# Kernel tuning notes

Measured on AMD Instinct MI355X. Metric: run time of the kernel, lower is better.

## Reference

```python
import jax, jax.numpy as jnp
import numpy as np

N_NODES = 100000
N_EDGES = 3200000
IN_DIM = 256
HID = 64
OUT_DIM = 1


def gcn_conv(x, W, b, src, dst, n):
    # PyG GCNConv: h = x @ W; add self loops; sym-normalize; aggregate; + b
    h = x @ W  # [N, F]
    # degrees include self loops (edge_weight = 1), computed on target nodes
    ones = jnp.ones(src.shape[0], dtype=x.dtype)
    deg = jax.ops.segment_sum(ones, dst, num_segments=n) + 1.0  # +1 for self loop
    dinv = jax.lax.rsqrt(deg)
    norm = dinv[src] * dinv[dst]  # [E]
    msg = h[src] * norm[:, None]  # gather + scale
    out = jax.ops.segment_sum(msg, dst, num_segments=n)
    # self-loop contribution: norm_ii = dinv[i]^2
    out = out + h * (dinv * dinv)[:, None]
    return out + b


def setup_inputs() -> dict:
    key = jax.random.key(0)
    ks = jax.random.split(key, 6)
    x = jax.random.normal(ks[0], (N_NODES, IN_DIM), dtype=jnp.float32)
    edge_index = jax.random.randint(ks[1], (2, N_EDGES), 0, N_NODES, dtype=jnp.int64)
    W1 = jax.random.normal(ks[2], (IN_DIM, HID), dtype=jnp.float32) / np.sqrt(IN_DIM)
    b1 = jnp.zeros((HID,), dtype=jnp.float32)
    W2 = jax.random.normal(ks[3], (HID, HID), dtype=jnp.float32) / np.sqrt(HID)
    b2 = jnp.zeros((HID,), dtype=jnp.float32)
    Wf = jax.random.normal(ks[4], (HID, OUT_DIM), dtype=jnp.float32) / np.sqrt(HID)
    bf = jnp.zeros((OUT_DIM,), dtype=jnp.float32)
    return {"x": x, "edge_index": edge_index, "W1": W1, "b1": b1,
            "W2": W2, "b2": b2, "Wf": Wf, "bf": bf}


def reference(x, edge_index, W1, b1, W2, b2, Wf, bf):
    src, dst = edge_index[0], edge_index[1]
    n = x.shape[0]
    h = jax.nn.relu(gcn_conv(x, W1, b1, src, dst, n))
    h = jax.nn.relu(gcn_conv(h, W2, b2, src, dst, n))
    g = jnp.mean(h, axis=0)  # [HID] graph readout
    return jax.nn.sigmoid(g @ Wf + bf)  # [OUT_DIM]
```

## Files before the change

### kernel.cpp

```cpp
#include <hip/hip_runtime.h>


typedef unsigned int u32;
typedef unsigned short u16;
typedef unsigned char u8;
typedef short s16x8 __attribute__((ext_vector_type(8)));
typedef __bf16 bf16x8 __attribute__((ext_vector_type(8)));
typedef float f32x4 __attribute__((ext_vector_type(4)));

constexpr int HID  = 64;
constexpr int SH   = 7;
constexpr int BK   = 128;
constexpr int BPAD = 1024;
constexpr int CH   = 4096;
constexpr int SLOT = 5120;
constexpr int NBLK2 = 4096;

static __device__ __forceinline__ u8 f2fp8(float f) {
    int p = __builtin_amdgcn_cvt_pk_fp8_f32(f, f, 0, false);
    return (u8)(p & 0xFF);
}
static __device__ __forceinline__ float fp82f(u8 v) {
    return __builtin_amdgcn_cvt_f32_fp8((int)v, 0);
}
static __device__ __forceinline__ u16 f2bf(float f) {
    u32 u = __float_as_uint(f);
    return (u16)((u + 0x7FFFu + ((u >> 16) & 1u)) >> 16);
}

__global__ void init_bcur_kernel(int* __restrict__ bcur, int B) {
    int b = blockIdx.x * 256 + threadIdx.x;
    if (b < B) bcur[b] = b * SLOT;
}

__global__ __launch_bounds__(256) void partition_kernel(const int* __restrict__ src,
                                                        const int* __restrict__ dst,
                                                        int* __restrict__ bcur,
                                                        u32* __restrict__ ep, int ne) {
    __shared__ int hcnt[BPAD];
    __shared__ int hoff[BPAD];
    __shared__ int gbase[BPAD];
    __shared__ u32 stage[CH];
    __shared__ int ssc[256];
    const int t = threadIdx.x;
    const int base = blockIdx.x * CH;
    const int cnt = min(CH, ne - base);
    for (int i = t; i < BPAD; i += 256) hcnt[i] = 0;
    __syncthreads();

    int myr[CH / 256];
    #pragma unroll
    for (int k = 0; k < CH / 256; ++k) {
        int i = t + k * 256;
        if (i < cnt) myr[k] = atomicAdd(&hcnt[dst[base + i] >> SH], 1);
    }
    __syncthreads();
    {
        int c0 = hcnt[t*4], c1 = hcnt[t*4+1], c2 = hcnt[t*4+2], c3 = hcnt[t*4+3];
        int tsum = c0 + c1 + c2 + c3;
        ssc[t] = tsum; __syncthreads();
        int run = tsum;
        for (int off = 1; off < 256; off <<= 1) {
            int v = (t >= off) ? ssc[t - off] : 0;
            __syncthreads();
            run += v; ssc[t] = run;
            __syncthreads();
        }
        int ex = run - tsum;
        hoff[t*4] = ex; ex += c0;
        hoff[t*4+1] = ex; ex += c1;
        hoff[t*4+2] = ex; ex += c2;
        hoff[t*4+3] = ex;
    }
    __syncthreads();
    for (int b = t; b < BPAD; b += 256) {
        int c = hcnt[b];
        if (c) gbase[b] = atomicAdd(&bcur[b], c);
    }
    #pragma unroll
    for (int k = 0; k < CH / 256; ++k) {
        int i = t + k * 256;
        if (i < cnt) {
            int s = src[base + i], d = dst[base + i];
            stage[hoff[d >> SH] + myr[k]] = ((u32)(d & (BK - 1)) << 20) | (u32)s;
        }
    }
    __syncthreads();
    for (int i = t; i < cnt; i += 256) {
        u32 v = stage[i];
        int lo = 0;
        #pragma unroll
        for (int s = 512; s; s >>= 1) {
            int m = lo + s;
            if (m < BPAD && hoff[m] <= i) lo = m;
        }
        ep[gbase[lo] + (i - hoff[lo])] = v;
    }
}

__global__ __launch_bounds__(256) void bucket_sort_kernel(const u32* __restrict__ ep,
                                                          const int* __restrict__ bcur,
                                                          int* __restrict__ eidx,
                                                          int* __restrict__ rowend,
                                                          float* __restrict__ dinv, int n) {
    __shared__ int cnt[BK];
    __shared__ int sc[BK];
    __shared__ int cur[BK];
    const int t = threadIdx.x, b = blockIdx.x;
    const int beg = b * SLOT, end = bcur[b];
    if (t < BK) cnt[t] = 0;
    __syncthreads();
    for (int p = beg + t; p < end; p += 256) atomicAdd(&cnt[ep[p] >> 20], 1);
    __syncthreads();
    if (t < BK) sc[t] = cnt[t];
    __syncthreads();
    for (int o = 1; o < BK; o <<= 1) {
        int v = 0;
        if (t < BK && t >= o) v = sc[t - o];
        __syncthreads();
        if (t < BK) sc[t] += v;
        __syncthreads();
    }
    if (t < BK) {
        int node = b * BK + t;
        if (node < n) {
            rowend[node] = beg + sc[t];
            dinv[node] = rsqrtf((float)cnt[t] + 1.0f);
        }
        cur[t] = beg + sc[t] - cnt[t];
    }
    __syncthreads();
    for (int p = beg + t; p < end; p += 256) {
        u32 v = ep[p];
        int r = atomicAdd(&cur[v >> 20], 1);
        eidx[r] = (int)(v & 0xFFFFFu);
    }
}

template <int K>
__global__ void pack_w_kernel(const float* __restrict__ W, u16* __restrict__ wpack) {
    int i = blockIdx.x * 256 + threadIdx.x;
    if (i >= K * 64) return;
    int e = i & 7, lane = (i >> 3) & 63, nt = (i >> 9) & 3, kk = i >> 11;
    int k = kk * 32 + (lane >> 4) * 8 + e;
    int c = nt * 16 + (lane & 15);
    wpack[i] = f2bf(W[k * HID + c]);
}

template <int K, typename TIn>
__global__ __launch_bounds__(256) void mfma_gemm_kernel(const TIn* __restrict__ A,
                                                        const u16* __restrict__ wpack,
                                                        const float* __restrict__ dinv,
                                                        u8* __restrict__ out8, int n) {
    const int t = threadIdx.x;
    const int lane = t & 63;
    const int wid = t >> 6;
    const int r16 = lane & 15;
    const int kgrp = lane >> 4;
    const int ntiles = (n + 15) >> 4;
    for (int tile = blockIdx.x * 4 + wid; tile < ntiles; tile += gridDim.x * 4) {
        const int row0 = tile * 16;
        const int arow = row0 + r16;
        f32x4 acc[4] = {f32x4{0,0,0,0}, f32x4{0,0,0,0}, f32x4{0,0,0,0}, f32x4{0,0,0,0}};
        #pragma unroll
        for (int kk = 0; kk < K / 32; ++kk) {
            s16x8 abits;
            if constexpr (sizeof(TIn) == 4) {
                const float* Af = (const float*)A;
                if (arow < n) {
                    const float4* p0 = (const float4*)(Af + (size_t)arow * K + kk * 32 + kgrp * 8);
                    float4 v0 = p0[0], v1 = p0[1];
                    abits[0] = (short)f2bf(v0.x); abits[1] = (short)f2bf(v0.y);
                    abits[2] = (short)f2bf(v0.z); abits[3] = (short)f2bf(v0.w);
                    abits[4] = (short)f2bf(v1.x); abits[5] = (short)f2bf(v1.y);
                    abits[6] = (short)f2bf(v1.z); abits[7] = (short)f2bf(v1.w);
                } else {
                    #pragma unroll
                    for (int j = 0; j < 8; ++j) abits[j] = 0;
                }
            } else {
                const u8* Ab = (const u8*)A;
                u32 w0 = 0, w1 = 0;
                if (arow < n) {
                    const u32* p0 = (const u32*)(Ab + (size_t)arow * K + kk * 32 + kgrp * 8);
                    w0 = p0[0]; w1 = p0[1];
                }
                abits[0] = (short)f2bf(__builtin_amdgcn_cvt_f32_fp8((int)w0, 0));
                abits[1] = (short)f2bf(__builtin_amdgcn_cvt_f32_fp8((int)w0, 1));
                abits[2] = (short)f2bf(__builtin_amdgcn_cvt_f32_fp8((int)w0, 2));
                abits[3] = (short)f2bf(__builtin_amdgcn_cvt_f32_fp8((int)w0, 3));
                abits[4] = (short)f2bf(__builtin_amdgcn_cvt_f32_fp8((int)w1, 0));
                abits[5] = (short)f2bf(__builtin_amdgcn_cvt_f32_fp8((int)w1, 1));
                abits[6] = (short)f2bf(__builtin_amdgcn_cvt_f32_fp8((int)w1, 2));
                abits[7] = (short)f2bf(__builtin_amdgcn_cvt_f32_fp8((int)w1, 3));
            }
            bf16x8 afrag = __builtin_bit_cast(bf16x8, abits);
            const u16* wp = wpack + ((size_t)(kk * 4) * 64 + lane) * 8;
            #pragma unroll
            for (int nt = 0; nt < 4; ++nt) {
                bf16x8 bfrag = *(const bf16x8*)(wp + (size_t)nt * 64 * 8);
                acc[nt] = __builtin_amdgcn_mfma_f32_16x16x32_bf16(afrag, bfrag, acc[nt], 0, 0, 0);
            }
        }
        #pragma unroll
        for (int reg = 0; reg < 4; ++reg) {
            int r = row0 + kgrp * 4 + reg;
            if (r < n) {
                float dv = dinv[r];
                #pragma unroll
                for (int nt = 0; nt < 4; ++nt)
                    out8[(size_t)r * HID + nt * 16 + r16] = f2fp8(acc[nt][reg] * dv);
            }
        }
    }
}

#define CVT4(acc0, acc1, acc2, acc3, wv) \
    acc0 += __builtin_amdgcn_cvt_f32_fp8((int)(wv), 0); \
    acc1 += __builtin_amdgcn_cvt_f32_fp8((int)(wv), 1); \
    acc2 += __builtin_amdgcn_cvt_f32_fp8((int)(wv), 2); \
    acc3 += __builtin_amdgcn_cvt_f32_fp8((int)(wv), 3);

__global__ __launch_bounds__(256) void agg_csr_kernel(const u8* __restrict__ hp,
                                                      const int* __restrict__ eidx,
                                                      const int* __restrict__ rowend,
                                                      const float* __restrict__ dinv,
                                                      const float* __restrict__ bias,
                                                      u8* __restrict__ out, int n) {
    int w = (blockIdx.x * 256 + threadIdx.x) >> 6;
    int lane = threadIdx.x & 63;
    if (w >= n) return;
    const int g = lane >> 4, fb = lane & 15;
    int beg = (w & (BK - 1)) ? rowend[w - 1] : (w >> SH) * SLOT;
    int end = rowend[w];
    float a0 = 0.f, a1 = 0.f, a2 = 0.f, a3 = 0.f;
    int p = beg;
    for (; p + 32 <= end; p += 32) {
        int s[8];
        #pragma unroll
        for (int j = 0; j < 8; ++j) s[j] = __builtin_nontemporal_load(eidx + p + j * 4 + g);
        u32 wv[8];
        #pragma unroll
        for (int j = 0; j < 8; ++j) wv[j] = *(const u32*)(hp + (size_t)s[j] * 64 + fb * 4);
        #pragma unroll
        for (int j = 0; j < 8; ++j) { CVT4(a0, a1, a2, a3, wv[j]) }
    }
    if (p + 16 <= end) {
        int s[4];
        #pragma unroll
        for (int j = 0; j < 4; ++j) s[j] = __builtin_nontemporal_load(eidx + p + j * 4 + g);
        u32 wv[4];
        #pragma unroll
        for (int j = 0; j < 4; ++j) wv[j] = *(const u32*)(hp + (size_t)s[j] * 64 + fb * 4);
        #pragma unroll
        for (int j = 0; j < 4; ++j) { CVT4(a0, a1, a2, a3, wv[j]) }
        p += 16;
    }
    for (; p < end; p += 4) {
        int idx = p + g;
        bool valid = idx < end;
        int s = __builtin_nontemporal_load(eidx + (valid ? idx : beg));
        u32 wv = *(const u32*)(hp + (size_t)s * 64 + fb * 4);
        if (valid) { CVT4(a0, a1, a2, a3, wv) }
    }
    a0 += __shfl_xor(a0, 16); a0 += __shfl_xor(a0, 32);
    a1 += __shfl_xor(a1, 16); a1 += __shfl_xor(a1, 32);
    a2 += __shfl_xor(a2, 16); a2 += __shfl_xor(a2, 32);
    a3 += __shfl_xor(a3, 16); a3 += __shfl_xor(a3, 32);
    u32 sv = *(const u32*)(hp + (size_t)w * 64 + fb * 4);
    float dv = dinv[w];
    float v0 = fmaxf(dv * (a0 + __builtin_amdgcn_cvt_f32_fp8((int)sv, 0)) + bias[fb * 4 + 0], 0.f);
    float v1 = fmaxf(dv * (a1 + __builtin_amdgcn_cvt_f32_fp8((int)sv, 1)) + bias[fb * 4 + 1], 0.f);
    float v2 = fmaxf(dv * (a2 + __builtin_amdgcn_cvt_f32_fp8((int)sv, 2)) + bias[fb * 4 + 2], 0.f);
    float v3 = fmaxf(dv * (a3 + __builtin_amdgcn_cvt_f32_fp8((int)sv, 3)) + bias[fb * 4 + 3], 0.f);
    if (g == 0) {
        int r = __builtin_amdgcn_cvt_pk_fp8_f32(v0, v1, 0, false);
        r = __builtin_amdgcn_cvt_pk_fp8_f32(v2, v3, r, true);
        *(u32*)(out + (size_t)w * 64 + fb * 4) = (u32)r;
    }
}

__global__ __launch_bounds__(256) void agg_csr_reduce_kernel(const u8* __restrict__ hp,
                                                             const int* __restrict__ eidx,
                                                             const int* __restrict__ rowend,
                                                             const float* __restrict__ dinv,
                                                             const float* __restrict__ bias,
                                                             float* __restrict__ partials, int n) {
    __shared__ float sred[256];
    int t = threadIdx.x, lane = t & 63;
    const int g = lane >> 4, fb = lane & 15;
    int wid = (blockIdx.x * 256 + t) >> 6;
    int wstride = gridDim.x * 4;
    float bl0 = bias[fb * 4 + 0], bl1 = bias[fb * 4 + 1];
    float bl2 = bias[fb * 4 + 2], bl3 = bias[fb * 4 + 3];
    float t0 = 0.f, t1 = 0.f, t2 = 0.f, t3 = 0.f;
    for (int w = wid; w < n; w += wstride) {
        int beg = (w & (BK - 1)) ? rowend[w - 1] : (w >> SH) * SLOT;
        int end = rowend[w];
        float a0 = 0.f, a1 = 0.f, a2 = 0.f, a3 = 0.f;
        int p = beg;
        for (; p + 32 <= end; p += 32) {
            int s[8];
            #pragma unroll
            for (int j = 0; j < 8; ++j) s[j] = __builtin_nontemporal_load(eidx + p + j * 4 + g);
            u32 wv[8];
            #pragma unroll
            for (int j = 0; j < 8; ++j) wv[j] = *(const u32*)(hp + (size_t)s[j] * 64 + fb * 4);
            #pragma unroll
            for (int j = 0; j < 8; ++j) { CVT4(a0, a1, a2, a3, wv[j]) }
        }
        if (p + 16 <= end) {
            int s[4];
            #pragma unroll
            for (int j = 0; j < 4; ++j) s[j] = __builtin_nontemporal_load(eidx + p + j * 4 + g);
            u32 wv[4];
            #pragma unroll
            for (int j = 0; j < 4; ++j) wv[j] = *(const u32*)(hp + (size_t)s[j] * 64 + fb * 4);
            #pragma unroll
            for (int j = 0; j < 4; ++j) { CVT4(a0, a1, a2, a3, wv[j]) }
            p += 16;
        }
        for (; p < end; p += 4) {
            int idx = p + g;
            bool valid = idx < end;
            int s = __builtin_nontemporal_load(eidx + (valid ? idx : beg));
            u32 wv = *(const u32*)(hp + (size_t)s * 64 + fb * 4);
            if (valid) { CVT4(a0, a1, a2, a3, wv) }
        }
        a0 += __shfl_xor(a0, 16); a0 += __shfl_xor(a0, 32);
        a1 += __shfl_xor(a1, 16); a1 += __shfl_xor(a1, 32);
        a2 += __shfl_xor(a2, 16); a2 += __shfl_xor(a2, 32);
        a3 += __shfl_xor(a3, 16); a3 += __shfl_xor(a3, 32);
        u32 sv = *(const u32*)(hp + (size_t)w * 64 + fb * 4);
        float dv = dinv[w];
        t0 += fmaxf(dv * (a0 + __builtin_amdgcn_cvt_f32_fp8((int)sv, 0)) + bl0, 0.f);
        t1 += fmaxf(dv * (a1 + __builtin_amdgcn_cvt_f32_fp8((int)sv, 1)) + bl1, 0.f);
        t2 += fmaxf(dv * (a2 + __builtin_amdgcn_cvt_f32_fp8((int)sv, 2)) + bl2, 0.f);
        t3 += fmaxf(dv * (a3 + __builtin_amdgcn_cvt_f32_fp8((int)sv, 3)) + bl3, 0.f);
    }
    int wv_ = t >> 6;
    if (g == 0) {
        sred[wv_ * 64 + fb * 4 + 0] = t0;
        sred[wv_ * 64 + fb * 4 + 1] = t1;
        sred[wv_ * 64 + fb * 4 + 2] = t2;
        sred[wv_ * 64 + fb * 4 + 3] = t3;
    }
    __syncthreads();
    if (t < 64) partials[blockIdx.x * 64 + t] = sred[t] + sred[t + 64] + sred[t + 128] + sred[t + 192];
}

__global__ __launch_bounds__(256) void gsum_stage_kernel(const float* __restrict__ parts, int nblk,
                                                         float* __restrict__ gsum) {
    __shared__ float sred[256];
    int t = threadIdx.x, col = t & 63;
    float a = 0.f;
    for (int bk = blockIdx.x * 4 + (t >> 6); bk < nblk; bk += gridDim.x * 4)
        a += parts[bk * 64 + col];
    sred[t] = a; __syncthreads();
    if (t < 64) atomicAdd(&gsum[t], sred[t] + sred[t + 64] + sred[t + 128] + sred[t + 192]);
}

__global__ void final_gsum_kernel(const float* __restrict__ gsum, const float* __restrict__ Wf,
                                  const float* __restrict__ bf_, float* __restrict__ out, float invn) {
    int lane = threadIdx.x;
    float v = gsum[lane] * invn * Wf[lane];
    #pragma unroll
    for (int off = 32; off; off >>= 1) v += __shfl_down(v, off);
    if (lane == 0) out[0] = 1.f / (1.f + expf(-(v + bf_[0])));
}

template <int K, typename TIn>
__global__ __launch_bounds__(256) void gemm_scale_kernel(const TIn* __restrict__ A,
                                                         const float* __restrict__ W,
                                                         const float* __restrict__ dinv,
                                                         u8* __restrict__ out8, int n) {
    __shared__ float xs[16][K];
    const int t = threadIdx.x;
    const int row0 = blockIdx.x * 16;
    if constexpr (sizeof(TIn) == 4) {
        const float* Af = (const float*)A;
        for (int i = t; i < 16 * K; i += 256) {
            int r = i / K;
            (&xs[0][0])[i] = (row0 + r < n) ? Af[(size_t)row0 * K + i] : 0.f;
        }
    } else {
        const u8* Ab = (const u8*)A;
        for (int i = t; i < 16 * K; i += 256) {
            int r = i / K;
            (&xs[0][0])[i] = (row0 + r < n) ? fp82f(Ab[(size_t)row0 * K + i]) : 0.f;
        }
    }
    __syncthreads();
    const int c = t & 63, rg = t >> 6;
    float acc[4] = {0.f, 0.f, 0.f, 0.f};
    #pragma unroll 4
    for (int k = 0; k < K; ++k) {
        float w = W[k * HID + c];
        #pragma unroll
        for (int j = 0; j < 4; ++j) acc[j] += xs[rg + 4 * j][k] * w;
    }
    #pragma unroll
    for (int j = 0; j < 4; ++j) {
        int r = row0 + rg + 4 * j;
        if (r < n) out8[(size_t)r * HID + c] = f2fp8(acc[j] * dinv[r]);
    }
}
__global__ void deg_f_kernel(const int* __restrict__ dst, float* __restrict__ deg, int ne) {
    int i = blockIdx.x * blockDim.x + threadIdx.x, st = gridDim.x * blockDim.x;
    for (; i < ne; i += st) atomicAdd(&deg[dst[i]], 1.0f);
}
__global__ void dinvf_kernel(float* __restrict__ deg, int n) {
    int i = blockIdx.x * blockDim.x + threadIdx.x;
    if (i < n) deg[i] = rsqrtf(deg[i] + 1.0f);
}
__global__ __launch_bounds__(256) void aggregate_atomic_kernel(const u8* __restrict__ hp,
        const int* __restrict__ src, const int* __restrict__ dst,
        const float* __restrict__ dinv, float* __restrict__ outf, int ne) {
    size_t tt = (size_t)blockIdx.x * 256 + threadIdx.x;
    int e = (int)(tt >> 6), f = (int)(tt & 63);
    if (e >= ne) return;
    int s = src[e], d = dst[e];
    atomicAdd(&outf[(size_t)d * HID + f], fp82f(hp[s * HID + f]) * dinv[d]);
}
__global__ void finalize1_fb_kernel(u8* __restrict__ hp, const float* __restrict__ agg,
                                    const float* __restrict__ dinv, const float* __restrict__ b, int n) {
    size_t i = (size_t)blockIdx.x * blockDim.x + threadIdx.x;
    if (i >= (size_t)n * HID) return;
    int node = (int)(i >> 6);
    float v = agg[i] + fp82f(hp[i]) * dinv[node] + b[i & 63];
    hp[i] = f2fp8(fmaxf(v, 0.f));
}
__global__ __launch_bounds__(256) void finalize2_fb_kernel(const u8* __restrict__ hp,
        const float* __restrict__ agg, const float* __restrict__ dinv,
        const float* __restrict__ b, float* __restrict__ gsum, int n) {
    __shared__ float sred[256];
    const int t = threadIdx.x, c = t & 63;
    const size_t total = (size_t)n * HID;
    const size_t stride = (size_t)gridDim.x * blockDim.x;
    float acc = 0.f;
    for (size_t i = (size_t)blockIdx.x * blockDim.x + t; i < total; i += stride) {
        int node = (int)(i >> 6);
        acc += fmaxf(agg[i] + fp82f(hp[i]) * dinv[node] + b[c], 0.f);
    }
    sred[t] = acc; __syncthreads();
    if (t < 64) atomicAdd(&gsum[c], sred[t] + sred[t + 64] + sred[t + 128] + sred[t + 192]);
}
__global__ void final_gsum_fb_kernel(const float* __restrict__ gsum, const float* __restrict__ Wf,
                                     const float* __restrict__ bf_, float* __restrict__ out, int n) {
    int lane = threadIdx.x;
    float v = (gsum[lane] / (float)n) * Wf[lane];
    #pragma unroll
    for (int off = 32; off; off >>= 1) v += __shfl_down(v, off);
    if (lane == 0) out[0] = 1.f / (1.f + expf(-(v + bf_[0])));
}

extern "C" void kernel_launch(void* const* d_in, const int* in_sizes, int n_in,
                              void* d_out, int out_size, void* d_ws, size_t ws_size,
                              hipStream_t stream) {
    const float* x  = (const float*)d_in[0];
    const int*   ei = (const int*)d_in[1];
    const float* W1 = (const float*)d_in[2];
    const float* b1 = (const float*)d_in[3];
    const float* W2 = (const float*)d_in[4];
    const float* b2 = (const float*)d_in[5];
    const float* Wf = (const float*)d_in[6];
    const float* bf_ = (const float*)d_in[7];
    float* out = (float*)d_out;

    const int n  = in_sizes[0] / 256;
    const int ne = in_sizes[1] / 2;
    const int* srcp = ei;
    const int* dstp = ei + ne;
    const int B = (n + BK - 1) / BK;

    char* p = (char*)d_ws;
    u32*   ep     = (u32*)p;   p += ((size_t)B * SLOT + 4096) * 4;
    int*   bcur   = (int*)p;   p += BPAD * 4;
    float* dinv   = (float*)p; p += (size_t)n * 4;
    int*   rowend = (int*)p;   p += (size_t)n * 4;
    float* gsum   = (float*)p; p += 64 * 4;
    int*   eidx   = (int*)p;   p += ((size_t)B * SLOT + 4096) * 4;
    float* parts  = (float*)p; p += (size_t)NBLK2 * 64 * 4;
    p = (char*)(((uintptr_t)p + 15) & ~(uintptr_t)15);
    u16*   wpack1 = (u16*)p;   p += 256 * 64 * 2;
    u16*   wpack2 = (u16*)p;   p += 64 * 64 * 2;
    u8*    hp     = (u8*)p;    p += (size_t)n * HID;
    u8*    h1     = (u8*)p;    p += (size_t)n * HID;
    size_t need = (size_t)(p - (char*)d_ws);

    bool slack_ok = ((size_t)ne / (size_t)B) <= (size_t)(SLOT - 1024);

    if (ws_size >= need && n <= (1 << 17) && slack_ok) {
        (void)hipMemsetAsync(gsum, 0, 64 * 4, stream);
        init_bcur_kernel<<<(B + 255) / 256, 256, 0, stream>>>(bcur, B);
        partition_kernel<<<(ne + CH - 1) / CH, 256, 0, stream>>>(srcp, dstp, bcur, ep, ne);
        bucket_sort_kernel<<<B, 256, 0, stream>>>(ep, bcur, eidx, rowend, dinv, n);
        pack_w_kernel<256><<<64, 256, 0, stream>>>(W1, wpack1);
        pack_w_kernel<64><<<16, 256, 0, stream>>>(W2, wpack2);

        const int ntiles = (n + 15) / 16;
        const int gblk = (ntiles + 3) / 4;
        mfma_gemm_kernel<256, float><<<gblk, 256, 0, stream>>>(x, wpack1, dinv, hp, n);
        agg_csr_kernel<<<(n + 3) / 4, 256, 0, stream>>>(hp, eidx, rowend, dinv, b1, h1, n);
        mfma_gemm_kernel<64, u8><<<gblk, 256, 0, stream>>>(h1, wpack2, dinv, hp, n);
        agg_csr_reduce_kernel<<<NBLK2, 256, 0, stream>>>(hp, eidx, rowend, dinv, b2, parts, n);
        gsum_stage_kernel<<<128, 256, 0, stream>>>(parts, NBLK2, gsum);
        final_gsum_kernel<<<1, 64, 0, stream>>>(gsum, Wf, bf_, out, 1.0f / (float)n);
    } else {
        char* q = (char*)d_ws;
        float* dinvF = (float*)q; q += (size_t)n * 4;
        float* gsumF = (float*)q; q += 64 * 4;
        u8*    hpF   = (u8*)q;   q += (size_t)n * HID;
        float* aggF  = (float*)q;

        (void)hipMemsetAsync(dinvF, 0, ((size_t)n + 64) * 4, stream);
        deg_f_kernel<<<2048, 256, 0, stream>>>(dstp, dinvF, ne);
        dinvf_kernel<<<(n + 255) / 256, 256, 0, stream>>>(dinvF, n);

        gemm_scale_kernel<256, float><<<(n + 15) / 16, 256, 0, stream>>>(x, W1, dinvF, hpF, n);
        (void)hipMemsetAsync(aggF, 0, (size_t)n * HID * 4, stream);
        aggregate_atomic_kernel<<<(int)(((size_t)ne * 64 + 255) / 256), 256, 0, stream>>>(hpF, srcp, dstp, dinvF, aggF, ne);
        finalize1_fb_kernel<<<(int)(((size_t)n * HID + 255) / 256), 256, 0, stream>>>(hpF, aggF, dinvF, b1, n);

        gemm_scale_kernel<64, u8><<<(n + 15) / 16, 256, 0, stream>>>(hpF, W2, dinvF, hpF, n);
        (void)hipMemsetAsync(aggF, 0, (size_t)n * HID * 4, stream);
        aggregate_atomic_kernel<<<(int)(((size_t)ne * 64 + 255) / 256), 256, 0, stream>>>(hpF, srcp, dstp, dinvF, aggF, ne);
        finalize2_fb_kernel<<<2048, 256, 0, stream>>>(hpF, aggF, dinvF, b2, gsumF, n);
        final_gsum_fb_kernel<<<1, 64, 0, stream>>>(gsumF, Wf, bf_, out, n);
    }
}
```

Measured before the change: 267.9 us.

## Split feature matrices into two 32-column halves and aggregate each half separately

The hidden features are stored as two separate 32-byte-per-node FP8 arrays, and each aggregation pass runs twice, once per half. This shrinks the gathered working set of each pass (3.2 MB instead of 6.4 MB) so the random neighbor gathers fit better in cache. The trade-off is reading the CSR edge indices twice, launching extra kernels, and issuing 32-byte gathers that use less of each cache line. The GEMM kernels and the reduction stage are adapted to read and write the split layout.

```diff
diff --git a/kernel.cpp b/kernel.cpp
--- a/kernel.cpp
+++ b/kernel.cpp
@@ -149,9 +149,11 @@
 
 template <int K, typename TIn>
 __global__ __launch_bounds__(256) void mfma_gemm_kernel(const TIn* __restrict__ A,
+                                                        const TIn* __restrict__ A2,
                                                         const u16* __restrict__ wpack,
                                                         const float* __restrict__ dinv,
-                                                        u8* __restrict__ out8, int n) {
+                                                        u8* __restrict__ outA,
+                                                        u8* __restrict__ outB, int n) {
     const int t = threadIdx.x;
     const int lane = t & 63;
     const int wid = t >> 6;
@@ -179,10 +181,10 @@
                     for (int j = 0; j < 8; ++j) abits[j] = 0;
                 }
             } else {
-                const u8* Ab = (const u8*)A;
+                const u8* src = (kk == 0) ? (const u8*)A : (const u8*)A2;
                 u32 w0 = 0, w1 = 0;
                 if (arow < n) {
-                    const u32* p0 = (const u32*)(Ab + (size_t)arow * K + kk * 32 + kgrp * 8);
+                    const u32* p0 = (const u32*)(src + (size_t)arow * 32 + kgrp * 8);
                     w0 = p0[0]; w1 = p0[1];
                 }
                 abits[0] = (short)f2bf(__builtin_amdgcn_cvt_f32_fp8((int)w0, 0));
@@ -208,8 +210,10 @@
             if (r < n) {
                 float dv = dinv[r];
                 #pragma unroll
-                for (int nt = 0; nt < 4; ++nt)
-                    out8[(size_t)r * HID + nt * 16 + r16] = f2fp8(acc[nt][reg] * dv);
+                for (int nt = 0; nt < 4; ++nt) {
+                    u8* o = (nt < 2) ? outA : outB;
+                    o[(size_t)r * 32 + (nt & 1) * 16 + r16] = f2fp8(acc[nt][reg] * dv);
+                }
             }
         }
     }
@@ -221,78 +225,67 @@
     acc2 += __builtin_amdgcn_cvt_f32_fp8((int)(wv), 2); \
     acc3 += __builtin_amdgcn_cvt_f32_fp8((int)(wv), 3);
 
-__global__ __launch_bounds__(256) void agg_csr_kernel(const u8* __restrict__ hp,
-                                                      const int* __restrict__ eidx,
-                                                      const int* __restrict__ rowend,
-                                                      const float* __restrict__ dinv,
-                                                      const float* __restrict__ bias,
-                                                      u8* __restrict__ out, int n) {
+__global__ __launch_bounds__(256) void agg_half_kernel(const u8* __restrict__ hpH,
+                                                       const int* __restrict__ eidx,
+                                                       const int* __restrict__ rowend,
+                                                       const float* __restrict__ dinv,
+                                                       const float* __restrict__ biasH,
+                                                       u8* __restrict__ outH, int n) {
     int w = (blockIdx.x * 256 + threadIdx.x) >> 6;
     int lane = threadIdx.x & 63;
     if (w >= n) return;
-    const int g = lane >> 4, fb = lane & 15;
+    const int g = lane >> 3, fb = lane & 7;
     int beg = (w & (BK - 1)) ? rowend[w - 1] : (w >> SH) * SLOT;
     int end = rowend[w];
     float a0 = 0.f, a1 = 0.f, a2 = 0.f, a3 = 0.f;
     int p = beg;
     for (; p + 32 <= end; p += 32) {
-        int s[8];
-        #pragma unroll
-        for (int j = 0; j < 8; ++j) s[j] = __builtin_nontemporal_load(eidx + p + j * 4 + g);
-        u32 wv[8];
-        #pragma unroll
-        for (int j = 0; j < 8; ++j) wv[j] = *(const u32*)(hp + (size_t)s[j] * 64 + fb * 4);
-        #pragma unroll
-        for (int j = 0; j < 8; ++j) { CVT4(a0, a1, a2, a3, wv[j]) }
-    }
-    if (p + 16 <= end) {
         int s[4];
         #pragma unroll
-        for (int j = 0; j < 4; ++j) s[j] = __builtin_nontemporal_load(eidx + p + j * 4 + g);
+        for (int j = 0; j < 4; ++j) s[j] = __builtin_nontemporal_load(eidx + p + j * 8 + g);
         u32 wv[4];
         #pragma unroll
-        for (int j = 0; j < 4; ++j) wv[j] = *(const u32*)(hp + (size_t)s[j] * 64 + fb * 4);
+        for (int j = 0; j < 4; ++j) wv[j] = *(const u32*)(hpH + (size_t)s[j] * 32 + fb * 4);
         #pragma unroll
         for (int j = 0; j < 4; ++j) { CVT4(a0, a1, a2, a3, wv[j]) }
-        p += 16;
-    }
-    for (; p < end; p += 4) {
+    }
+    for (; p < end; p += 8) {
         int idx = p + g;
         bool valid = idx < end;
         int s = __builtin_nontemporal_load(eidx + (valid ? idx : beg));
-        u32 wv = *(const u32*)(hp + (size_t)s * 64 + fb * 4);
+        u32 wv = *(const u32*)(hpH + (size_t)s * 32 + fb * 4);
         if (valid) { CVT4(a0, a1, a2, a3, wv) }
     }
-    a0 += __shfl_xor(a0, 16); a0 += __shfl_xor(a0, 32);
-    a1 += __shfl_xor(a1, 16); a1 += __shfl_xor(a1, 32);
-    a2 += __shfl_xor(a2, 16); a2 += __shfl_xor(a2, 32);
-    a3 += __shfl_xor(a3, 16); a3 += __shfl_xor(a3, 32);
-    u32 sv = *(const u32*)(hp + (size_t)w * 64 + fb * 4);
+    a0 += __shfl_xor(a0, 8); a0 += __shfl_xor(a0, 16); a0 += __shfl_xor(a0, 32);
+    a1 += __shfl_xor(a1, 8); a1 += __shfl_xor(a1, 16); a1 += __shfl_xor(a1, 32);
+    a2 += __shfl_xor(a2, 8); a2 += __shfl_xor(a2, 16); a2 += __shfl_xor(a2, 32);
+    a3 += __shfl_xor(a3, 8); a3 += __shfl_xor(a3, 16); a3 += __shfl_xor(a3, 32);
+    u32 sv = *(const u32*)(hpH + (size_t)w * 32 + fb * 4);
     float dv = dinv[w];
-    float v0 = fmaxf(dv * (a0 + __builtin_amdgcn_cvt_f32_fp8((int)sv, 0)) + bias[fb * 4 + 0], 0.f);
-    float v1 = fmaxf(dv * (a1 + __builtin_amdgcn_cvt_f32_fp8((int)sv, 1)) + bias[fb * 4 + 1], 0.f);
-    float v2 = fmaxf(dv * (a2 + __builtin_amdgcn_cvt_f32_fp8((int)sv, 2)) + bias[fb * 4 + 2], 0.f);
-    float v3 = fmaxf(dv * (a3 + __builtin_amdgcn_cvt_f32_fp8((int)sv, 3)) + bias[fb * 4 + 3], 0.f);
+    float v0 = fmaxf(dv * (a0 + __builtin_amdgcn_cvt_f32_fp8((int)sv, 0)) + biasH[fb * 4 + 0], 0.f);
+    float v1 = fmaxf(dv * (a1 + __builtin_amdgcn_cvt_f32_fp8((int)sv, 1)) + biasH[fb * 4 + 1], 0.f);
+    float v2 = fmaxf(dv * (a2 + __builtin_amdgcn_cvt_f32_fp8((int)sv, 2)) + biasH[fb * 4 + 2], 0.f);
+    float v3 = fmaxf(dv * (a3 + __builtin_amdgcn_cvt_f32_fp8((int)sv, 3)) + biasH[fb * 4 + 3], 0.f);
     if (g == 0) {
         int r = __builtin_amdgcn_cvt_pk_fp8_f32(v0, v1, 0, false);
         r = __builtin_amdgcn_cvt_pk_fp8_f32(v2, v3, r, true);
-        *(u32*)(out + (size_t)w * 64 + fb * 4) = (u32)r;
-    }
-}
-
-__global__ __launch_bounds__(256) void agg_csr_reduce_kernel(const u8* __restrict__ hp,
-                                                             const int* __restrict__ eidx,
-                                                             const int* __restrict__ rowend,
-                                                             const float* __restrict__ dinv,
-                                                             const float* __restrict__ bias,
-                                                             float* __restrict__ partials, int n) {
-    __shared__ float sred[256];
+        __builtin_nontemporal_store((u32)r, (u32*)(outH + (size_t)w * 32 + fb * 4));
+    }
+}
+
+__global__ __launch_bounds__(256) void agg_reduce_half_kernel(const u8* __restrict__ hpH,
+                                                              const int* __restrict__ eidx,
+                                                              const int* __restrict__ rowend,
+                                                              const float* __restrict__ dinv,
+                                                              const float* __restrict__ biasH,
+                                                              float* __restrict__ partialsH, int n) {
+    __shared__ float sred[128];
     int t = threadIdx.x, lane = t & 63;
-    const int g = lane >> 4, fb = lane & 15;
+    const int g = lane >> 3, fb = lane & 7;
     int wid = (blockIdx.x * 256 + t) >> 6;
     int wstride = gridDim.x * 4;
-    float bl0 = bias[fb * 4 + 0], bl1 = bias[fb * 4 + 1];
-    float bl2 = bias[fb * 4 + 2], bl3 = bias[fb * 4 + 3];
+    float bl0 = biasH[fb * 4 + 0], bl1 = biasH[fb * 4 + 1];
+    float bl2 = biasH[fb * 4 + 2], bl3 = biasH[fb * 4 + 3];
     float t0 = 0.f, t1 = 0.f, t2 = 0.f, t3 = 0.f;
     for (int w = wid; w < n; w += wstride) {
         int beg = (w & (BK - 1)) ? rowend[w - 1] : (w >> SH) * SLOT;
@@ -300,38 +293,27 @@
         float a0 = 0.f, a1 = 0.f, a2 = 0.f, a3 = 0.f;
         int p = beg;
         for (; p + 32 <= end; p += 32) {
-            int s[8];
-            #pragma unroll
-            for (int j = 0; j < 8; ++j) s[j] = __builtin_nontemporal_load(eidx + p + j * 4 + g);
-            u32 wv[8];
-            #pragma unroll
-            for (int j = 0; j < 8; ++j) wv[j] = *(const u32*)(hp + (size_t)s[j] * 64 + fb * 4);
-            #pragma unroll
-            for (int j = 0; j < 8; ++j) { CVT4(a0, a1, a2, a3, wv[j]) }
-        }
-        if (p + 16 <= end) {
             int s[4];
             #pragma unroll
-            for (int j = 0; j < 4; ++j) s[j] = __builtin_nontemporal_load(eidx + p + j * 4 + g);
+            for (int j = 0; j < 4; ++j) s[j] = __builtin_nontemporal_load(eidx + p + j * 8 + g);
             u32 wv[4];
             #pragma unroll
-            for (int j = 0; j < 4; ++j) wv[j] = *(const u32*)(hp + (size_t)s[j] * 64 + fb * 4);
+            for (int j = 0; j < 4; ++j) wv[j] = *(const u32*)(hpH + (size_t)s[j] * 32 + fb * 4);
             #pragma unroll
             for (int j = 0; j < 4; ++j) { CVT4(a0, a1, a2, a3, wv[j]) }
-            p += 16;
-        }
-        for (; p < end; p += 4) {
+        }
+        for (; p < end; p += 8) {
             int idx = p + g;
             bool valid = idx < end;
             int s = __builtin_nontemporal_load(eidx + (valid ? idx : beg));
-            u32 wv = *(const u32*)(hp + (size_t)s * 64 + fb * 4);
+            u32 wv = *(const u32*)(hpH + (size_t)s * 32 + fb * 4);
             if (valid) { CVT4(a0, a1, a2, a3, wv) }
         }
-        a0 += __shfl_xor(a0, 16); a0 += __shfl_xor(a0, 32);
-        a1 += __shfl_xor(a1, 16); a1 += __shfl_xor(a1, 32);
-        a2 += __shfl_xor(a2, 16); a2 += __shfl_xor(a2, 32);
-        a3 += __shfl_xor(a3, 16); a3 += __shfl_xor(a3, 32);
-        u32 sv = *(const u32*)(hp + (size_t)w * 64 + fb * 4);
+        a0 += __shfl_xor(a0, 8); a0 += __shfl_xor(a0, 16); a0 += __shfl_xor(a0, 32);
+        a1 += __shfl_xor(a1, 8); a1 += __shfl_xor(a1, 16); a1 += __shfl_xor(a1, 32);
+        a2 += __shfl_xor(a2, 8); a2 += __shfl_xor(a2, 16); a2 += __shfl_xor(a2, 32);
+        a3 += __shfl_xor(a3, 8); a3 += __shfl_xor(a3, 16); a3 += __shfl_xor(a3, 32);
+        u32 sv = *(const u32*)(hpH + (size_t)w * 32 + fb * 4);
         float dv = dinv[w];
         t0 += fmaxf(dv * (a0 + __builtin_amdgcn_cvt_f32_fp8((int)sv, 0)) + bl0, 0.f);
         t1 += fmaxf(dv * (a1 + __builtin_amdgcn_cvt_f32_fp8((int)sv, 1)) + bl1, 0.f);
@@ -340,22 +322,25 @@
     }
     int wv_ = t >> 6;
     if (g == 0) {
-        sred[wv_ * 64 + fb * 4 + 0] = t0;
-        sred[wv_ * 64 + fb * 4 + 1] = t1;
-        sred[wv_ * 64 + fb * 4 + 2] = t2;
-        sred[wv_ * 64 + fb * 4 + 3] = t3;
-    }
-    __syncthreads();
-    if (t < 64) partials[blockIdx.x * 64 + t] = sred[t] + sred[t + 64] + sred[t + 128] + sred[t + 192];
-}
-
-__global__ __launch_bounds__(256) void gsum_stage_kernel(const float* __restrict__ parts, int nblk,
+        sred[wv_ * 32 + fb * 4 + 0] = t0;
+        sred[wv_ * 32 + fb * 4 + 1] = t1;
+        sred[wv_ * 32 + fb * 4 + 2] = t2;
+        sred[wv_ * 32 + fb * 4 + 3] = t3;
+    }
+    __syncthreads();
+    if (t < 32) partialsH[blockIdx.x * 32 + t] = sred[t] + sred[t + 32] + sred[t + 64] + sred[t + 96];
+}
+
+__global__ __launch_bounds__(256) void gsum_stage_kernel(const float* __restrict__ partsA,
+                                                         const float* __restrict__ partsB, int nblk,
                                                          float* __restrict__ gsum) {
     __shared__ float sred[256];
     int t = threadIdx.x, col = t & 63;
+    const float* ps = (col < 32) ? partsA : partsB;
+    int c32 = col & 31;
     float a = 0.f;
     for (int bk = blockIdx.x * 4 + (t >> 6); bk < nblk; bk += gridDim.x * 4)
-        a += parts[bk * 64 + col];
+        a += ps[bk * 32 + c32];
     sred[t] = a; __syncthreads();
     if (t < 64) atomicAdd(&gsum[t], sred[t] + sred[t + 64] + sred[t + 128] + sred[t + 192]);
 }
@@ -480,12 +465,15 @@
     int*   rowend = (int*)p;   p += (size_t)n * 4;
     float* gsum   = (float*)p; p += 64 * 4;
     int*   eidx   = (int*)p;   p += ((size_t)B * SLOT + 4096) * 4;
-    float* parts  = (float*)p; p += (size_t)NBLK2 * 64 * 4;
+    float* partsA = (float*)p; p += (size_t)NBLK2 * 32 * 4;
+    float* partsB = (float*)p; p += (size_t)NBLK2 * 32 * 4;
     p = (char*)(((uintptr_t)p + 15) & ~(uintptr_t)15);
     u16*   wpack1 = (u16*)p;   p += 256 * 64 * 2;
     u16*   wpack2 = (u16*)p;   p += 64 * 64 * 2;
-    u8*    hp     = (u8*)p;    p += (size_t)n * HID;
-    u8*    h1     = (u8*)p;    p += (size_t)n * HID;
+    u8*    hpA    = (u8*)p;    p += (size_t)n * 32;
+    u8*    hpB    = (u8*)p;    p += (size_t)n * 32;
+    u8*    h1A    = (u8*)p;    p += (size_t)n * 32;
+    u8*    h1B    = (u8*)p;    p += (size_t)n * 32;
     size_t need = (size_t)(p - (char*)d_ws);
 
     bool slack_ok = ((size_t)ne / (size_t)B) <= (size_t)(SLOT - 1024);
@@ -500,11 +488,14 @@
 
         const int ntiles = (n + 15) / 16;
         const int gblk = (ntiles + 3) / 4;
-        mfma_gemm_kernel<256, float><<<gblk, 256, 0, stream>>>(x, wpack1, dinv, hp, n);
-        agg_csr_kernel<<<(n + 3) / 4, 256, 0, stream>>>(hp, eidx, rowend, dinv, b1, h1, n);
-        mfma_gemm_kernel<64, u8><<<gblk, 256, 0, stream>>>(h1, wpack2, dinv, hp, n);
-        agg_csr_reduce_kernel<<<NBLK2, 256, 0, stream>>>(hp, eidx, rowend, dinv, b2, parts, n);
-        gsum_stage_kernel<<<128, 256, 0, stream>>>(parts, NBLK2, gsum);
+        const int ablk = (n + 3) / 4;
+        mfma_gemm_kernel<256, float><<<gblk, 256, 0, stream>>>(x, nullptr, wpack1, dinv, hpA, hpB, n);
+        agg_half_kernel<<<ablk, 256, 0, stream>>>(hpA, eidx, rowend, dinv, b1, h1A, n);
+        agg_half_kernel<<<ablk, 256, 0, stream>>>(hpB, eidx, rowend, dinv, b1 + 32, h1B, n);
+        mfma_gemm_kernel<64, u8><<<gblk, 256, 0, stream>>>(h1A, h1B, wpack2, dinv, hpA, hpB, n);
+        agg_reduce_half_kernel<<<NBLK2, 256, 0, stream>>>(hpA, eidx, rowend, dinv, b2, partsA, n);
+        agg_reduce_half_kernel<<<NBLK2, 256, 0, stream>>>(hpB, eidx, rowend, dinv, b2 + 32, partsB, n);
+        gsum_stage_kernel<<<128, 256, 0, stream>>>(partsA, partsB, NBLK2, gsum);
         final_gsum_kernel<<<1, 64, 0, stream>>>(gsum, Wf, bf_, out, 1.0f / (float)n);
     } else {
         char* q = (char*)d_ws;
```

After: 322.4 us. 1.2x slower.
